# Kernel optimization log

Measured on AMD Instinct MI355X. Metric: run time of the kernel, lower is better.

## Reference

```python
import jax, jax.numpy as jnp
import numpy as np

STD = 0.1  # hidden-state noise std (module's self.std)
T, B, I, H = 2048, 256, 64, 128


def setup_inputs() -> dict:
    key = jax.random.key(0)
    k = jax.random.split(key, 5)
    x = jax.random.normal(k[0], (T, B, I), dtype=jnp.float32)
    # xavier-ish input weights, orthogonal-ish recurrent weights (init_weights analogue)
    w_ih = jax.random.normal(k[1], (H, I), dtype=jnp.float32) * np.float32(1.0 / np.sqrt(I))
    a = jax.random.normal(k[2], (H, H), dtype=jnp.float32)
    q, _ = jnp.linalg.qr(a)
    w_hh = q.astype(jnp.float32)
    b_ih = jnp.zeros((H,), jnp.float32)
    b_hh = jnp.zeros((H,), jnp.float32)
    noise = jax.random.normal(k[3], (T, B, H), dtype=jnp.float32)  # per-step randn
    hidden_in = jnp.zeros((1, B, H), jnp.float32)
    return {"x": x, "w_ih": w_ih, "w_hh": w_hh, "b_ih": b_ih, "b_hh": b_hh,
            "noise": noise, "hidden_in": hidden_in}


def reference(x, w_ih, w_hh, b_ih, b_hh, noise, hidden_in):
    # torch nn.RNN (tanh) step: h_t = tanh(W_ih x_t + b_ih + W_hh h_{t-1} + b_hh)
    # noiseRNN noisy branch: after emitting out_t = h_t, hidden += std * randn
    xw = jnp.einsum('tbi,hi->tbh', x, w_ih) + b_ih  # one big GEMM for input proj

    def step(h, inp):
        xw_t, n_t = inp
        h_new = jnp.tanh(xw_t + h @ w_hh.T + b_hh)   # [B,H]
        h_next = h_new + STD * n_t                    # noise injected into carried state
        return h_next, h_new

    h0 = hidden_in[0]                                 # [B,H]
    h_last, outs = jax.lax.scan(step, h0, (xw, noise))
    return outs, h_last[None]                         # ([T,B,H], [1,B,H])
```

## Files before the change

### kernel.cpp

```cpp
#include <hip/hip_runtime.h>


constexpr int T_ = 2048;
constexpr int B_ = 256;
constexpr int I_ = 64;
constexpr int H_ = 128;
constexpr int BH_ = B_ * H_;
constexpr int BI_ = B_ * I_;
constexpr long long TBH_ = (long long)T_ * BH_;
constexpr float STD_ = 0.1f;
constexpr int AUG_ = H_ + I_;
constexpr int JPT_ = AUG_ / 4;

__global__ __launch_bounds__(256)
void rnn_scan(const float* __restrict__ x, const float* __restrict__ w_ih,
              const float* __restrict__ w_hh, const float* __restrict__ b_ih,
              const float* __restrict__ b_hh, const float* __restrict__ noise,
              const float* __restrict__ h0, float* __restrict__ out)
{
    __shared__ float aug[2][AUG_];
    __shared__ float part[4 * 132];

    const int b   = blockIdx.x;
    const int tid = threadIdx.x;
    const int q   = tid >> 6;
    const int h2  = tid & 63;
    const int j0  = q * JPT_;

    float W0[JPT_], W1[JPT_];
#pragma unroll
    for (int jj = 0; jj < JPT_; ++jj) {
        const int j = j0 + jj;
        if (j < H_) {
            W0[jj] = w_hh[h2 * H_ + j];
            W1[jj] = w_hh[(h2 + 64) * H_ + j];
        } else {
            W0[jj] = w_ih[h2 * I_ + (j - H_)];
            W1[jj] = w_ih[(h2 + 64) * I_ + (j - H_)];
        }
    }

    float bias = 0.0f;
    if (tid < H_) bias = b_ih[tid] + b_hh[tid];

    if (tid < H_) aug[0][tid] = h0[b * H_ + tid];
    if (tid < I_) aug[0][H_ + tid] = x[b * I_ + tid];
    __syncthreads();

    int p = 0;
    for (int t = 0; t < T_; ++t) {
        float nv = 0.0f, xv = 0.0f;
        if (tid < H_) nv = noise[(long long)t * BH_ + b * H_ + tid];
        if (tid < I_ && (t + 1) < T_) xv = x[(long long)(t + 1) * BI_ + b * I_ + tid];

        float p0 = 0.0f, p1 = 0.0f;
        const float* ap = &aug[p][j0];
#pragma unroll
        for (int i = 0; i < JPT_ / 4; ++i) {
            const float4 v = *(const float4*)(ap + 4 * i);
            p0 = fmaf(v.x, W0[4 * i + 0], p0);  p1 = fmaf(v.x, W1[4 * i + 0], p1);
            p0 = fmaf(v.y, W0[4 * i + 1], p0);  p1 = fmaf(v.y, W1[4 * i + 1], p1);
            p0 = fmaf(v.z, W0[4 * i + 2], p0);  p1 = fmaf(v.z, W1[4 * i + 2], p1);
            p0 = fmaf(v.w, W0[4 * i + 3], p0);  p1 = fmaf(v.w, W1[4 * i + 3], p1);
        }
        part[q * 132 + h2]      = p0;
        part[q * 132 + h2 + 64] = p1;
        __syncthreads();

        const int np = p ^ 1;
        if (tid < H_) {
            const float s = part[tid] + part[132 + tid] + part[264 + tid]
                          + part[396 + tid] + bias;
            const float hn = tanhf(s);
            out[(long long)t * BH_ + b * H_ + tid] = hn;
            const float hnx = fmaf(STD_, nv, hn);
            aug[np][tid] = hnx;
            if (t == T_ - 1) out[TBH_ + b * H_ + tid] = hnx;
        }
        if (tid < I_) aug[np][H_ + tid] = xv;
        __syncthreads();
        p = np;
    }
}

extern "C" void kernel_launch(void* const* d_in, const int* in_sizes, int n_in,
                              void* d_out, int out_size, void* d_ws, size_t ws_size,
                              hipStream_t stream) {
    const float* x     = (const float*)d_in[0];
    const float* w_ih  = (const float*)d_in[1];
    const float* w_hh  = (const float*)d_in[2];
    const float* b_ih  = (const float*)d_in[3];
    const float* b_hh  = (const float*)d_in[4];
    const float* noise = (const float*)d_in[5];
    const float* h0    = (const float*)d_in[6];
    float* outp        = (float*)d_out;

    rnn_scan<<<dim3(B_), dim3(256), 0, stream>>>(x, w_ih, w_hh, b_ih, b_hh,
                                                 noise, h0, outp);
}
```

Before: 1.770 ms.

## Use one barrier per RNN step with redundant reduction, prefetching, and fast tanh

The per-step schedule is restructured so that all four waves redundantly reduce the partial sums and write the full next-state vector. The `part` buffer is double-buffered so that a single raw `s_barrier`, waiting only on LDS (`lgkmcnt`), replaces two `__syncthreads` per step. Noise and x loads are prefetched two to three steps ahead in registers. Rows are interleaved so each thread handles adjacent outputs with float2 accesses. `tanhf` is replaced with an exp-based fast approximation, which trades some accuracy for fewer instructions on the serial critical path.

```diff
diff --git a/kernel.cpp b/kernel.cpp
--- a/kernel.cpp
+++ b/kernel.cpp
@@ -11,20 +11,29 @@
 constexpr float STD_ = 0.1f;
 constexpr int AUG_ = H_ + I_;
 constexpr int JPT_ = AUG_ / 4;
+constexpr int PSTR_ = 132;
 
-__global__ __launch_bounds__(256)
+__device__ __forceinline__ float tanh_fast(float s) {
+    const float e = __expf(2.0f * s);
+    return 1.0f - __fdividef(2.0f, e + 1.0f);
+}
+
+#define BAR() asm volatile("s_waitcnt lgkmcnt(0)\n\ts_barrier" ::: "memory")
+
+__global__ __launch_bounds__(256, 1)
 void rnn_scan(const float* __restrict__ x, const float* __restrict__ w_ih,
               const float* __restrict__ w_hh, const float* __restrict__ b_ih,
               const float* __restrict__ b_hh, const float* __restrict__ noise,
               const float* __restrict__ h0, float* __restrict__ out)
 {
-    __shared__ float aug[2][AUG_];
-    __shared__ float part[4 * 132];
+    __shared__ __align__(16) float aug[2][AUG_];
+    __shared__ __align__(16) float part[2][4 * PSTR_];
 
     const int b   = blockIdx.x;
     const int tid = threadIdx.x;
     const int q   = tid >> 6;
-    const int h2  = tid & 63;
+    const int l   = tid & 63;
+    const int r0  = 2 * l;
     const int j0  = q * JPT_;
 
     float W0[JPT_], W1[JPT_];
@@ -32,26 +41,36 @@
     for (int jj = 0; jj < JPT_; ++jj) {
         const int j = j0 + jj;
         if (j < H_) {
-            W0[jj] = w_hh[h2 * H_ + j];
-            W1[jj] = w_hh[(h2 + 64) * H_ + j];
+            W0[jj] = w_hh[r0 * H_ + j];
+            W1[jj] = w_hh[(r0 + 1) * H_ + j];
         } else {
-            W0[jj] = w_ih[h2 * I_ + (j - H_)];
-            W1[jj] = w_ih[(h2 + 64) * I_ + (j - H_)];
+            W0[jj] = w_ih[r0 * I_ + (j - H_)];
+            W1[jj] = w_ih[(r0 + 1) * I_ + (j - H_)];
         }
     }
 
-    float bias = 0.0f;
-    if (tid < H_) bias = b_ih[tid] + b_hh[tid];
+    const float bias0 = b_ih[r0] + b_hh[r0];
+    const float bias1 = b_ih[r0 + 1] + b_hh[r0 + 1];
 
-    if (tid < H_) aug[0][tid] = h0[b * H_ + tid];
-    if (tid < I_) aug[0][H_ + tid] = x[b * I_ + tid];
-    __syncthreads();
+    {
+        const float2 h00 = *(const float2*)&h0[b * H_ + r0];
+        *(float2*)&aug[0][r0] = h00;
+        aug[0][H_ + l] = x[b * I_ + l];
+    }
 
-    int p = 0;
+    float2 nv_c = *(const float2*)&noise[(long long)0 * BH_ + b * H_ + r0];
+    float2 nv_n = *(const float2*)&noise[(long long)1 * BH_ + b * H_ + r0];
+    float  xv_c = x[(long long)1 * BI_ + b * I_ + l];
+    float  xv_n = x[(long long)2 * BI_ + b * I_ + l];
+
     for (int t = 0; t < T_; ++t) {
-        float nv = 0.0f, xv = 0.0f;
-        if (tid < H_) nv = noise[(long long)t * BH_ + b * H_ + tid];
-        if (tid < I_ && (t + 1) < T_) xv = x[(long long)(t + 1) * BI_ + b * I_ + tid];
+        const int p  = t & 1;
+        const int np = p ^ 1;
+
+        float2 nv_f = make_float2(0.0f, 0.0f);
+        float  xv_f = 0.0f;
+        if (t + 2 < T_) nv_f = *(const float2*)&noise[(long long)(t + 2) * BH_ + b * H_ + r0];
+        if (t + 3 < T_) xv_f = x[(long long)(t + 3) * BI_ + b * I_ + l];
 
         float p0 = 0.0f, p1 = 0.0f;
         const float* ap = &aug[p][j0];
@@ -63,23 +82,32 @@
             p0 = fmaf(v.z, W0[4 * i + 2], p0);  p1 = fmaf(v.z, W1[4 * i + 2], p1);
             p0 = fmaf(v.w, W0[4 * i + 3], p0);  p1 = fmaf(v.w, W1[4 * i + 3], p1);
         }
-        part[q * 132 + h2]      = p0;
-        part[q * 132 + h2 + 64] = p1;
-        __syncthreads();
+        *(float2*)&part[p][q * PSTR_ + r0] = make_float2(p0, p1);
 
-        const int np = p ^ 1;
-        if (tid < H_) {
-            const float s = part[tid] + part[132 + tid] + part[264 + tid]
-                          + part[396 + tid] + bias;
-            const float hn = tanhf(s);
-            out[(long long)t * BH_ + b * H_ + tid] = hn;
-            const float hnx = fmaf(STD_, nv, hn);
-            aug[np][tid] = hnx;
-            if (t == T_ - 1) out[TBH_ + b * H_ + tid] = hnx;
-        }
-        if (tid < I_) aug[np][H_ + tid] = xv;
-        __syncthreads();
-        p = np;
+        BAR();
+
+        const float2 a0 = *(const float2*)&part[p][0 * PSTR_ + r0];
+        const float2 a1 = *(const float2*)&part[p][1 * PSTR_ + r0];
+        const float2 a2 = *(const float2*)&part[p][2 * PSTR_ + r0];
+        const float2 a3 = *(const float2*)&part[p][3 * PSTR_ + r0];
+        const float s0 = (a0.x + a1.x) + (a2.x + a3.x) + bias0;
+        const float s1 = (a0.y + a1.y) + (a2.y + a3.y) + bias1;
+        const float hn0 = tanh_fast(s0);
+        const float hn1 = tanh_fast(s1);
+
+        if (q == 0)
+            *(float2*)&out[(long long)t * BH_ + b * H_ + r0] = make_float2(hn0, hn1);
+
+        const float hx0 = fmaf(STD_, nv_c.x, hn0);
+        const float hx1 = fmaf(STD_, nv_c.y, hn1);
+        *(float2*)&aug[np][r0] = make_float2(hx0, hx1);
+        aug[np][H_ + l] = xv_c;
+
+        if (t == T_ - 1 && q == 0)
+            *(float2*)&out[TBH_ + b * H_ + r0] = make_float2(hx0, hx1);
+
+        nv_c = nv_n; nv_n = nv_f;
+        xv_c = xv_n; xv_n = xv_f;
     }
 }
 
```

After: 1.599 ms. 1.11x faster.
